# Performance work log

Hardware: AMD Instinct MI355X
Metric: run time of the kernel (lower is better)

Reference implementation:

```python
import jax, jax.numpy as jnp
import numpy as np

N, D = 8192, 256
SIM_THRESHOLD = 0.85
EPS = 1e-12  # matches torch F.normalize eps


def setup_inputs() -> dict:
    key = jax.random.key(0)
    k1, k2, k3 = jax.random.split(key, 3)
    return {
        "cls_embeddings": jax.random.normal(k1, (N, D), dtype=jnp.float32),
        "w1": jax.random.normal(k2, (4, 16), dtype=jnp.float32) * 0.5,
        "b1": jnp.zeros((16,), dtype=jnp.float32),
        "w2": jax.random.normal(k3, (16, 1), dtype=jnp.float32) * 0.25,
        "b2": jnp.zeros((1,), dtype=jnp.float32),
    }


def _similarity_features(cls_embeddings):
    # 4-dim features from the pairwise cosine-similarity matrix.
    n = cls_embeddings.shape[0]
    norm = jnp.maximum(jnp.linalg.norm(cls_embeddings, axis=-1, keepdims=True), EPS)
    normed = cls_embeddings / norm
    sim = normed @ normed.T                      # [n, n]
    eye = jnp.eye(n, dtype=bool)
    off = ~eye
    n_pairs = n * (n - 1)
    max_sim = jnp.where(off, sim, -jnp.inf).max()
    mean_sim = jnp.where(off, sim, 0.0).sum() / n_pairs
    frac_above = (jnp.where(off, sim, 0.0) > SIM_THRESHOLD).sum() / n_pairs

    # Connected components over edges {sim > 0.85} == union-find cluster count.
    # Min-label propagation + pointer jumping (Shiloach-Vishkin style),
    # converges in O(log n) iterations.
    adj = (jax.lax.stop_gradient(sim) > SIM_THRESHOLD) | eye  # include self
    labels0 = jnp.arange(n, dtype=jnp.int32)

    def body(_, labels):
        nb_min = jnp.where(adj, labels[None, :], n).min(axis=1).astype(jnp.int32)
        labels = jnp.minimum(labels, nb_min)
        return labels[labels]  # pointer jump

    iters = int(np.ceil(np.log2(max(n, 2)))) + 3
    labels = jax.lax.fori_loop(0, iters, body, labels0)
    cluster_count = (labels == labels0).sum() / n  # roots are component minima

    return jnp.stack([max_sim, mean_sim,
                      frac_above.astype(jnp.float32),
                      cluster_count.astype(jnp.float32)])


def reference(cls_embeddings, w1, b1, w2, b2):
    feats = _similarity_features(cls_embeddings)[None, :]          # [1, 4]
    h = jax.nn.gelu(feats @ w1 + b1, approximate=False)            # [1, 16]
    score = jax.nn.sigmoid(h @ w2 + b2)                            # [1, 1]
    return score
```

## Files before the change

kernel.cpp:

```cpp
#include <hip/hip_runtime.h>
#include <math.h>

#define NROWS 8192
#define DIM   256
#define K2    512
#define NTB   64
#define SIM_THR 0.85f

#define A2_OFF   1024
#define EDGE_OFF (1024 + NROWS * K2 * 2)

typedef _Float16 half8 __attribute__((ext_vector_type(8)));
typedef float f32x4 __attribute__((ext_vector_type(4)));

__device__ inline void load_lds16(const void* g, void* l) {
    __builtin_amdgcn_global_load_lds((const __attribute__((address_space(1))) void*)g,
                                     (__attribute__((address_space(3))) void*)l, 16, 0, 0);
}

__device__ inline void atomicMaxF(float* addr, float val) {
    if (val >= 0.f) atomicMax((int*)addr, __float_as_int(val));
    else            atomicMin((unsigned int*)addr, __float_as_uint(val));
}

__global__ __launch_bounds__(256) void prep_kernel(const float* __restrict__ x,
                                                   unsigned short* __restrict__ a2,
                                                   float* wsf) {
    if (blockIdx.x == 0 && threadIdx.x == 0) {
        wsf[0] = -INFINITY; wsf[1] = 0.f;
        ((unsigned int*)wsf)[2] = 0u; ((unsigned int*)wsf)[3] = 0u;
    }
    int row  = blockIdx.x * 4 + (threadIdx.x >> 6);
    int lane = threadIdx.x & 63;
    float4 v = ((const float4*)(x + (size_t)row * DIM))[lane];
    float ss = v.x * v.x + v.y * v.y + v.z * v.z + v.w * v.w;
    #pragma unroll
    for (int off = 32; off; off >>= 1) ss += __shfl_xor(ss, off);
    float norm = fmaxf(sqrtf(ss), 1e-12f);
    float f[4] = {v.x / norm, v.y / norm, v.z / norm, v.w / norm};
    unsigned short h[4], l[4];
    #pragma unroll
    for (int j = 0; j < 4; ++j) {
        _Float16 hh = (_Float16)f[j];
        _Float16 ll = (_Float16)(f[j] - (float)hh);
        h[j] = __builtin_bit_cast(unsigned short, hh);
        l[j] = __builtin_bit_cast(unsigned short, ll);
    }
    unsigned short* rp = a2 + (size_t)row * K2;
    *(ushort4*)(rp + lane * 4)       = make_ushort4(h[0], h[1], h[2], h[3]);
    *(ushort4*)(rp + DIM + lane * 4) = make_ushort4(l[0], l[1], l[2], l[3]);
}

__global__ __launch_bounds__(256) void sim_kernel(const unsigned short* __restrict__ a2,
                                                  float* wsf, int2* edges, int cap) {
    int idx = blockIdx.x;
    int bi = (int)((sqrtf(8.f * idx + 1.f) - 1.f) * 0.5f);
    while ((bi + 1) * (bi + 2) / 2 <= idx) ++bi;
    while (bi * (bi + 1) / 2 > idx) --bi;
    int bj = idx - bi * (bi + 1) / 2;
    int i0 = bi * 128, j0 = bj * 128;

    __shared__ __align__(16) char As[128 * 128];
    __shared__ __align__(16) char Bs[128 * 128];
    __shared__ float sred[12];

    int t = threadIdx.x, lane = t & 63, w = t >> 6;
    int wr = w >> 1, wc = w & 1;

    f32x4 acc[4][4] = {};

    int perm = ((lane & 7) ^ (lane >> 3)) * 16;
    const char* gA = (const char*)(a2 + (size_t)(i0 + w * 32 + (lane >> 3)) * K2) + perm;
    const char* gB = (const char*)(a2 + (size_t)(j0 + w * 32 + (lane >> 3)) * K2) + perm;
    char* lA = As + w * 32 * 128;
    char* lB = Bs + w * 32 * 128;

    int rbA = (wr * 64 + (lane & 15)) * 128;
    int rbB = (wc * 64 + (lane & 15)) * 128;
    int kx  = (lane & 7) << 4;
    int kb0 = (lane >> 4) * 16;

    for (int kc = 0; kc < 1024; kc += 128) {
        #pragma unroll
        for (int q = 0; q < 4; ++q) {
            load_lds16(gA + kc + q * 8192, lA + q * 1024);
            load_lds16(gB + kc + q * 8192, lB + q * 1024);
        }
        __syncthreads();

        #pragma unroll
        for (int ks = 0; ks < 2; ++ks) {
            int kb = ks * 64 + kb0;
            half8 af[4], bf[4];
            #pragma unroll
            for (int m = 0; m < 4; ++m) {
                af[m] = *(const half8*)(As + rbA + m * 2048 + (kb ^ kx));
                bf[m] = *(const half8*)(Bs + rbB + m * 2048 + (kb ^ kx));
            }
            #pragma unroll
            for (int m = 0; m < 4; ++m)
                #pragma unroll
                for (int n = 0; n < 4; ++n)
                    acc[m][n] = __builtin_amdgcn_mfma_f32_16x16x32_f16(af[m], bf[n], acc[m][n], 0, 0, 0);
        }
        __syncthreads();
    }

    bool diagT = (bi == bj);
    float        wgt  = diagT ? 1.f : 2.f;
    unsigned int wgtu = diagT ? 1u : 2u;
    float lmax = -INFINITY, lsum = 0.f;
    unsigned int lcnt = 0;
    #pragma unroll
    for (int m = 0; m < 4; ++m) {
        #pragma unroll
        for (int n = 0; n < 4; ++n) {
            #pragma unroll
            for (int j = 0; j < 4; ++j) {
                float s = acc[m][n][j];
                int gi = i0 + wr * 64 + m * 16 + (lane >> 4) * 4 + j;
                int gj = j0 + wc * 64 + n * 16 + (lane & 15);
                if (gi != gj) {
                    lmax = fmaxf(lmax, s);
                    lsum += s;
                    if (s > SIM_THR) {
                        lcnt++;
                        unsigned int e = atomicAdd(&((unsigned int*)wsf)[3], 1u);
                        if (e < (unsigned int)cap) edges[e] = make_int2(gi, gj);
                    }
                }
            }
        }
    }
    #pragma unroll
    for (int off = 32; off; off >>= 1) {
        lmax = fmaxf(lmax, __shfl_xor(lmax, off));
        lsum += __shfl_xor(lsum, off);
        lcnt += __shfl_xor(lcnt, off);
    }
    if (lane == 0) { sred[w] = lmax; sred[4 + w] = lsum; ((unsigned int*)sred)[8 + w] = lcnt; }
    __syncthreads();
    if (t == 0) {
        float bm = fmaxf(fmaxf(sred[0], sred[1]), fmaxf(sred[2], sred[3]));
        float bs = sred[4] + sred[5] + sred[6] + sred[7];
        unsigned int bc = ((unsigned int*)sred)[8] + ((unsigned int*)sred)[9]
                        + ((unsigned int*)sred)[10] + ((unsigned int*)sred)[11];
        atomicMaxF(&wsf[0], bm);
        atomicAdd(&wsf[1], bs * wgt);
        if (bc) atomicAdd(&((unsigned int*)wsf)[2], bc * wgtu);
    }
}

__global__ __launch_bounds__(1024) void finalize_kernel(const float* wsf, const int2* edges, int cap,
                                                        const float* __restrict__ w1,
                                                        const float* __restrict__ b1,
                                                        const float* __restrict__ w2,
                                                        const float* __restrict__ b2,
                                                        float* __restrict__ out) {
    __shared__ int lab[NROWS];
    __shared__ int tmp[NROWS];
    __shared__ int wsum[16];
    int t = threadIdx.x;
    for (int i = t; i < NROWS; i += 1024) lab[i] = i;
    unsigned int ec = ((const unsigned int*)wsf)[3];
    if (ec > (unsigned int)cap) ec = (unsigned int)cap;
    __syncthreads();

    if (ec > 0) {
        for (int it = 0; it < 16; ++it) {
            for (int i = t; i < NROWS; i += 1024) tmp[i] = lab[i];
            __syncthreads();
            for (unsigned int e = t; e < ec; e += 1024) {
                int u = edges[e].x, v = edges[e].y;
                atomicMin(&tmp[u], lab[v]);
                atomicMin(&tmp[v], lab[u]);
            }
            __syncthreads();
            for (int i = t; i < NROWS; i += 1024) lab[i] = tmp[tmp[i]];
            __syncthreads();
        }
    }

    int lc = 0;
    for (int i = t; i < NROWS; i += 1024) lc += (lab[i] == i);
    #pragma unroll
    for (int off = 32; off; off >>= 1) lc += __shfl_xor(lc, off);
    if ((t & 63) == 0) wsum[t >> 6] = lc;
    __syncthreads();

    if (t == 0) {
        int roots = 0;
        #pragma unroll
        for (int q = 0; q < 16; ++q) roots += wsum[q];
        const float n_pairs = 67100672.0f;
        float feats[4];
        feats[0] = wsf[0];
        feats[1] = wsf[1] / n_pairs;
        feats[2] = (float)((const unsigned int*)wsf)[2] / n_pairs;
        feats[3] = (float)roots / (float)NROWS;
        float acc2 = b2[0];
        for (int j = 0; j < 16; ++j) {
            float hj = b1[j];
            #pragma unroll
            for (int i = 0; i < 4; ++i) hj = fmaf(feats[i], w1[i * 16 + j], hj);
            float g = 0.5f * hj * (1.0f + erff(hj * 0.70710678118f));
            acc2 = fmaf(g, w2[j], acc2);
        }
        out[0] = 1.0f / (1.0f + expf(-acc2));
    }
}

extern "C" void kernel_launch(void* const* d_in, const int* in_sizes, int n_in,
                              void* d_out, int out_size, void* d_ws, size_t ws_size,
                              hipStream_t stream) {
    const float* cls = (const float*)d_in[0];
    const float* w1  = (const float*)d_in[1];
    const float* b1  = (const float*)d_in[2];
    const float* w2  = (const float*)d_in[3];
    const float* b2  = (const float*)d_in[4];
    float* out = (float*)d_out;

    float* wsf = (float*)d_ws;
    unsigned short* a2 = (unsigned short*)((char*)d_ws + A2_OFF);
    int2* edges = (int2*)((char*)d_ws + EDGE_OFF);
    long long avail = (long long)ws_size - (long long)EDGE_OFF;
    int cap = (int)(avail > 0 ? (avail / 8 > 4194304 ? 4194304 : avail / 8) : 0);

    prep_kernel<<<NROWS / 4, 256, 0, stream>>>(cls, a2, wsf);
    sim_kernel<<<NTB * (NTB + 1) / 2, 256, 0, stream>>>(a2, wsf, edges, cap);
    finalize_kernel<<<1, 1024, 0, stream>>>(wsf, edges, cap, w1, b1, w2, b2, out);
}
```

Baseline: 151.2 us.

## Enlarge similarity tiles to 256x256 with 8 waves and double-buffered LDS loads

```diff
diff --git a/kernel.cpp b/kernel.cpp
--- a/kernel.cpp
+++ b/kernel.cpp
@@ -4,7 +4,7 @@
 #define NROWS 8192
 #define DIM   256
 #define K2    512
-#define NTB   64
+#define NTB   32
 #define SIM_THR 0.85f
 
 #define A2_OFF   1024
@@ -51,59 +51,69 @@
     *(ushort4*)(rp + DIM + lane * 4) = make_ushort4(l[0], l[1], l[2], l[3]);
 }
 
-__global__ __launch_bounds__(256) void sim_kernel(const unsigned short* __restrict__ a2,
-                                                  float* wsf, int2* edges, int cap) {
+__global__ __launch_bounds__(512, 2) void sim_kernel(const unsigned short* __restrict__ a2,
+                                                     float* wsf, int2* edges, int cap) {
     int idx = blockIdx.x;
     int bi = (int)((sqrtf(8.f * idx + 1.f) - 1.f) * 0.5f);
     while ((bi + 1) * (bi + 2) / 2 <= idx) ++bi;
     while (bi * (bi + 1) / 2 > idx) --bi;
     int bj = idx - bi * (bi + 1) / 2;
-    int i0 = bi * 128, j0 = bj * 128;
-
-    __shared__ __align__(16) char As[128 * 128];
-    __shared__ __align__(16) char Bs[128 * 128];
-    __shared__ float sred[12];
+    int i0 = bi * 256, j0 = bj * 256;
+
+    __shared__ __align__(16) char As[2][256 * 128];
+    __shared__ __align__(16) char Bs[2][256 * 128];
+    __shared__ float sred[24];
 
     int t = threadIdx.x, lane = t & 63, w = t >> 6;
-    int wr = w >> 1, wc = w & 1;
-
-    f32x4 acc[4][4] = {};
+    int wr = w >> 2, wc = w & 3;
+
+    f32x4 acc[8][4] = {};
 
     int perm = ((lane & 7) ^ (lane >> 3)) * 16;
-    const char* gA = (const char*)(a2 + (size_t)(i0 + w * 32 + (lane >> 3)) * K2) + perm;
-    const char* gB = (const char*)(a2 + (size_t)(j0 + w * 32 + (lane >> 3)) * K2) + perm;
-    char* lA = As + w * 32 * 128;
-    char* lB = Bs + w * 32 * 128;
-
-    int rbA = (wr * 64 + (lane & 15)) * 128;
-    int rbB = (wc * 64 + (lane & 15)) * 128;
+    const char* gA = (const char*)a2 + (size_t)(i0 + w * 32 + (lane >> 3)) * 1024 + perm;
+    const char* gB = (const char*)a2 + (size_t)(j0 + w * 32 + (lane >> 3)) * 1024 + perm;
+    int ldsW = w * 32 * 128;
+
+    int rbA = (wr * 128 + (lane & 15)) * 128;
+    int rbB = (wc * 64  + (lane & 15)) * 128;
     int kx  = (lane & 7) << 4;
-    int kb0 = (lane >> 4) * 16;
-
-    for (int kc = 0; kc < 1024; kc += 128) {
-        #pragma unroll
-        for (int q = 0; q < 4; ++q) {
-            load_lds16(gA + kc + q * 8192, lA + q * 1024);
-            load_lds16(gB + kc + q * 8192, lB + q * 1024);
-        }
-        __syncthreads();
-
+    int kb0 = (lane >> 4) << 4;
+
+    #pragma unroll
+    for (int q = 0; q < 4; ++q) {
+        load_lds16(gA + q * 8192, As[0] + ldsW + q * 1024);
+        load_lds16(gB + q * 8192, Bs[0] + ldsW + q * 1024);
+    }
+    __syncthreads();
+
+    int cur = 0;
+    for (int it = 0; it < 8; ++it) {
+        if (it < 7) {
+            int kc = (it + 1) * 128;
+            #pragma unroll
+            for (int q = 0; q < 4; ++q) {
+                load_lds16(gA + kc + q * 8192, As[cur ^ 1] + ldsW + q * 1024);
+                load_lds16(gB + kc + q * 8192, Bs[cur ^ 1] + ldsW + q * 1024);
+            }
+        }
+        const char* A = As[cur];
+        const char* B = Bs[cur];
         #pragma unroll
         for (int ks = 0; ks < 2; ++ks) {
-            int kb = ks * 64 + kb0;
-            half8 af[4], bf[4];
-            #pragma unroll
-            for (int m = 0; m < 4; ++m) {
-                af[m] = *(const half8*)(As + rbA + m * 2048 + (kb ^ kx));
-                bf[m] = *(const half8*)(Bs + rbB + m * 2048 + (kb ^ kx));
-            }
-            #pragma unroll
-            for (int m = 0; m < 4; ++m)
+            int kb = (ks * 64 + kb0) ^ kx;
+            half8 af[8], bf[4];
+            #pragma unroll
+            for (int m = 0; m < 8; ++m) af[m] = *(const half8*)(A + rbA + m * 2048 + kb);
+            #pragma unroll
+            for (int n = 0; n < 4; ++n) bf[n] = *(const half8*)(B + rbB + n * 2048 + kb);
+            #pragma unroll
+            for (int m = 0; m < 8; ++m)
                 #pragma unroll
                 for (int n = 0; n < 4; ++n)
                     acc[m][n] = __builtin_amdgcn_mfma_f32_16x16x32_f16(af[m], bf[n], acc[m][n], 0, 0, 0);
         }
         __syncthreads();
+        cur ^= 1;
     }
 
     bool diagT = (bi == bj);
@@ -112,14 +122,14 @@
     float lmax = -INFINITY, lsum = 0.f;
     unsigned int lcnt = 0;
     #pragma unroll
-    for (int m = 0; m < 4; ++m) {
+    for (int m = 0; m < 8; ++m) {
         #pragma unroll
         for (int n = 0; n < 4; ++n) {
             #pragma unroll
             for (int j = 0; j < 4; ++j) {
                 float s = acc[m][n][j];
-                int gi = i0 + wr * 64 + m * 16 + (lane >> 4) * 4 + j;
-                int gj = j0 + wc * 64 + n * 16 + (lane & 15);
+                int gi = i0 + wr * 128 + m * 16 + (lane >> 4) * 4 + j;
+                int gj = j0 + wc * 64  + n * 16 + (lane & 15);
                 if (gi != gj) {
                     lmax = fmaxf(lmax, s);
                     lsum += s;
@@ -138,13 +148,17 @@
         lsum += __shfl_xor(lsum, off);
         lcnt += __shfl_xor(lcnt, off);
     }
-    if (lane == 0) { sred[w] = lmax; sred[4 + w] = lsum; ((unsigned int*)sred)[8 + w] = lcnt; }
+    if (lane == 0) { sred[w] = lmax; sred[8 + w] = lsum; ((unsigned int*)sred)[16 + w] = lcnt; }
     __syncthreads();
     if (t == 0) {
-        float bm = fmaxf(fmaxf(sred[0], sred[1]), fmaxf(sred[2], sred[3]));
-        float bs = sred[4] + sred[5] + sred[6] + sred[7];
-        unsigned int bc = ((unsigned int*)sred)[8] + ((unsigned int*)sred)[9]
-                        + ((unsigned int*)sred)[10] + ((unsigned int*)sred)[11];
+        float bm = -INFINITY, bs = 0.f;
+        unsigned int bc = 0;
+        #pragma unroll
+        for (int q = 0; q < 8; ++q) {
+            bm = fmaxf(bm, sred[q]);
+            bs += sred[8 + q];
+            bc += ((unsigned int*)sred)[16 + q];
+        }
         atomicMaxF(&wsf[0], bm);
         atomicAdd(&wsf[1], bs * wgt);
         if (bc) atomicAdd(&((unsigned int*)wsf)[2], bc * wgtu);
@@ -227,6 +241,6 @@
     int cap = (int)(avail > 0 ? (avail / 8 > 4194304 ? 4194304 : avail / 8) : 0);
 
     prep_kernel<<<NROWS / 4, 256, 0, stream>>>(cls, a2, wsf);
-    sim_kernel<<<NTB * (NTB + 1) / 2, 256, 0, stream>>>(a2, wsf, edges, cap);
+    sim_kernel<<<NTB * (NTB + 1) / 2, 512, 0, stream>>>(a2, wsf, edges, cap);
     finalize_kernel<<<1, 1024, 0, stream>>>(wsf, edges, cap, w1, b1, w2, b2, out);
 }
```

Result: faster. 138.0 us (-8.7%).

## Double-buffer LDS tiles with async prefetch and remap block order

Applied to the files above, without the earlier changes.

```diff
diff --git a/kernel.cpp b/kernel.cpp
--- a/kernel.cpp
+++ b/kernel.cpp
@@ -5,6 +5,7 @@
 #define DIM   256
 #define K2    512
 #define NTB   64
+#define NTRI  2080
 #define SIM_THR 0.85f
 
 #define A2_OFF   1024
@@ -51,17 +52,18 @@
     *(ushort4*)(rp + DIM + lane * 4) = make_ushort4(l[0], l[1], l[2], l[3]);
 }
 
-__global__ __launch_bounds__(256) void sim_kernel(const unsigned short* __restrict__ a2,
-                                                  float* wsf, int2* edges, int cap) {
-    int idx = blockIdx.x;
+__global__ __launch_bounds__(256, 2) void sim_kernel(const unsigned short* __restrict__ a2,
+                                                     float* wsf, int2* edges, int cap) {
+    int bid = blockIdx.x;
+    int idx = (bid & 7) * (NTRI / 8) + (bid >> 3);
     int bi = (int)((sqrtf(8.f * idx + 1.f) - 1.f) * 0.5f);
     while ((bi + 1) * (bi + 2) / 2 <= idx) ++bi;
     while (bi * (bi + 1) / 2 > idx) --bi;
     int bj = idx - bi * (bi + 1) / 2;
     int i0 = bi * 128, j0 = bj * 128;
 
-    __shared__ __align__(16) char As[128 * 128];
-    __shared__ __align__(16) char Bs[128 * 128];
+    __shared__ __align__(16) char As[2][128 * 128];
+    __shared__ __align__(16) char Bs[2][128 * 128];
     __shared__ float sred[12];
 
     int t = threadIdx.x, lane = t & 63, w = t >> 6;
@@ -70,32 +72,47 @@
     f32x4 acc[4][4] = {};
 
     int perm = ((lane & 7) ^ (lane >> 3)) * 16;
-    const char* gA = (const char*)(a2 + (size_t)(i0 + w * 32 + (lane >> 3)) * K2) + perm;
-    const char* gB = (const char*)(a2 + (size_t)(j0 + w * 32 + (lane >> 3)) * K2) + perm;
-    char* lA = As + w * 32 * 128;
-    char* lB = Bs + w * 32 * 128;
+    const char* gA = (const char*)a2 + (size_t)(i0 + w * 32 + (lane >> 3)) * 1024 + perm;
+    const char* gB = (const char*)a2 + (size_t)(j0 + w * 32 + (lane >> 3)) * 1024 + perm;
+    int ldsW = w * 32 * 128;
 
     int rbA = (wr * 64 + (lane & 15)) * 128;
     int rbB = (wc * 64 + (lane & 15)) * 128;
     int kx  = (lane & 7) << 4;
-    int kb0 = (lane >> 4) * 16;
-
-    for (int kc = 0; kc < 1024; kc += 128) {
-        #pragma unroll
-        for (int q = 0; q < 4; ++q) {
-            load_lds16(gA + kc + q * 8192, lA + q * 1024);
-            load_lds16(gB + kc + q * 8192, lB + q * 1024);
-        }
-        __syncthreads();
-
+    int kb0 = (lane >> 4) << 4;
+
+    #pragma unroll
+    for (int q = 0; q < 4; ++q) {
+        load_lds16(gA + q * 8192, As[0] + ldsW + q * 1024);
+        load_lds16(gB + q * 8192, Bs[0] + ldsW + q * 1024);
+    }
+
+    for (int it = 0; it < 8; ++it) {
+        int c = it & 1;
+        if (it < 7) {
+            int kc = (it + 1) * 128;
+            #pragma unroll
+            for (int q = 0; q < 4; ++q) {
+                load_lds16(gA + kc + q * 8192, As[c ^ 1] + ldsW + q * 1024);
+                load_lds16(gB + kc + q * 8192, Bs[c ^ 1] + ldsW + q * 1024);
+            }
+            asm volatile("s_waitcnt vmcnt(8)" ::: "memory");
+        } else {
+            asm volatile("s_waitcnt vmcnt(0)" ::: "memory");
+        }
+        __builtin_amdgcn_s_barrier();
+
+        const char* A = As[c];
+        const char* B = Bs[c];
+        __builtin_amdgcn_s_setprio(1);
         #pragma unroll
         for (int ks = 0; ks < 2; ++ks) {
-            int kb = ks * 64 + kb0;
+            int kb = (ks * 64 + kb0) ^ kx;
             half8 af[4], bf[4];
             #pragma unroll
             for (int m = 0; m < 4; ++m) {
-                af[m] = *(const half8*)(As + rbA + m * 2048 + (kb ^ kx));
-                bf[m] = *(const half8*)(Bs + rbB + m * 2048 + (kb ^ kx));
+                af[m] = *(const half8*)(A + rbA + m * 2048 + kb);
+                bf[m] = *(const half8*)(B + rbB + m * 2048 + kb);
             }
             #pragma unroll
             for (int m = 0; m < 4; ++m)
@@ -103,7 +120,8 @@
                 for (int n = 0; n < 4; ++n)
                     acc[m][n] = __builtin_amdgcn_mfma_f32_16x16x32_f16(af[m], bf[n], acc[m][n], 0, 0, 0);
         }
-        __syncthreads();
+        __builtin_amdgcn_s_setprio(0);
+        __builtin_amdgcn_s_barrier();
     }
 
     bool diagT = (bi == bj);
@@ -227,6 +245,6 @@
     int cap = (int)(avail > 0 ? (avail / 8 > 4194304 ? 4194304 : avail / 8) : 0);
 
     prep_kernel<<<NROWS / 4, 256, 0, stream>>>(cls, a2, wsf);
-    sim_kernel<<<NTB * (NTB + 1) / 2, 256, 0, stream>>>(a2, wsf, edges, cap);
+    sim_kernel<<<NTRI, 256, 0, stream>>>(a2, wsf, edges, cap);
     finalize_kernel<<<1, 1024, 0, stream>>>(wsf, edges, cap, w1, b1, w2, b2, out);
 }
```

New measurement: 150.5 us. About the same (-0.5%).
